# Kernel optimization log

Measured on AMD Instinct MI355X. Metric: run time of the kernel, lower is better.

Reference implementation:

```python
import jax, jax.numpy as jnp
import numpy as np
from jax.scipy.stats import norm

B, IN, H0, H1, OUT = 1024, 2048, 4096, 4096, 1000
EPS_CDF = 1e-5
DECAY = 0.01
NEG_SLOPE = 0.01  # LeakyReLU default slope


def setup_inputs() -> dict:
    key = jax.random.key(0)
    ks = iter(jax.random.split(key, 40))
    rn = lambda shp, s=1.0: s * jax.random.normal(next(ks), shp, dtype=jnp.float32)
    inp = {}
    inp['x'] = rn((B, IN))
    inp['z_w'] = rn((IN,), 0.02)
    for nm, (o, i) in zip(['0', '1', 'o'], [(H0, IN), (H1, H0), (OUT, H1)]):
        inp['w_mu' + nm] = rn((o, i), 0.02)
        inp['w_ls' + nm] = rn((o, i), 0.1) - 2.0  # log-sigma ~ -2 => sigma ~ 0.13
        inp['b_mu' + nm] = rn((o,), 0.02)
        inp['b_ls' + nm] = rn((o,), 0.1) - 2.0
        inp['eps_w' + nm] = rn((o, i))
        inp['eps_b' + nm] = rn((o,))
    inp['pfz0'] = jax.random.uniform(next(ks), (B, H0), dtype=jnp.float32)
    inp['pfz1'] = jax.random.uniform(next(ks), (B, H1), dtype=jnp.float32)
    inp['y'] = jax.random.randint(next(ks), (B,), 0, OUT, dtype=jnp.int32)
    inp['mz0'] = jax.random.randint(next(ks), (B, H0), 0, 2, dtype=jnp.int32)
    inp['mz1'] = jax.random.randint(next(ks), (B, H1), 0, 2, dtype=jnp.int32)
    inp['mask_mu0'] = jax.random.randint(next(ks), (H0,), 0, 2, dtype=jnp.int32)
    inp['mask_mu1'] = jax.random.randint(next(ks), (H1,), 0, 2, dtype=jnp.int32)
    inp['data_set_size'] = 60000
    return inp


def _bayes_layer(h, w_mu, w_ls, b_mu, b_ls, eps_w, eps_b, mz, mask_mu, pfz):
    sw = jnp.exp(w_ls)
    sb = jnp.exp(b_ls)
    w = w_mu + sw * eps_w          # reparameterized weight sample
    b = b_mu + sb * eps_b
    h = h @ w.T + b                # F.linear
    h = jnp.where(h >= 0, h, NEG_SLOPE * h)  # LeakyReLU
    mzf = mz.astype(h.dtype)
    m = mzf * mask_mu.astype(h.dtype)[None, :]   # [B, h]
    mult = m.shape[1] / (m.sum(1) + 1e-6)        # rescale multiplier per sample
    h = h * m * mult[:, None]
    # GFN forward-flow log-prob of the z-mask
    p = jnp.clip(pfz, 1e-6, 1.0 - 1e-6)
    flow = (mzf * jnp.log(p) + (1.0 - mzf) * jnp.log(1.0 - p)).sum()
    # Gaussian CDF likelihood of sampled weights/biases (finite-difference density)
    pw = norm.cdf(w + EPS_CDF, w_mu, sw) - norm.cdf(w - EPS_CDF, w_mu, sw)
    pb = norm.cdf(b + EPS_CDF, b_mu, sb) - norm.cdf(b - EPS_CDF, b_mu, sb)
    flow = flow + jnp.log(pw).sum() + jnp.log(pb).sum()
    return h, flow


def reference(x, z_w, w_mu0, w_ls0, b_mu0, b_ls0, eps_w0, eps_b0,
              w_mu1, w_ls1, b_mu1, b_ls1, eps_w1, eps_b1,
              w_muo, w_lso, b_muo, b_lso, eps_wo, eps_bo,
              pfz0, pfz1, y, mz0, mz1, mask_mu0, mask_mu1, data_set_size):
    loss = (x @ z_w).sum()  # total flow estimator Z
    h, f0 = _bayes_layer(x, w_mu0, w_ls0, b_mu0, b_ls0, eps_w0, eps_b0, mz0, mask_mu0, pfz0)
    loss = loss + f0
    h, f1 = _bayes_layer(h, w_mu1, w_ls1, b_mu1, b_ls1, eps_w1, eps_b1, mz1, mask_mu1, pfz1)
    loss = loss + f1
    # output BayesLinear (sampled)
    wo = w_muo + jnp.exp(w_lso) * eps_wo
    bo = b_muo + jnp.exp(b_lso) * eps_bo
    pred = h @ wo.T + bo  # [B, OUT]
    logp = jax.nn.log_softmax(pred, axis=-1)
    ce = -jnp.take_along_axis(logp, y[:, None].astype(jnp.int32), axis=1).mean()
    loss = loss + jnp.float32(data_set_size) * ce  # NLL
    wd = DECAY * ((w_mu0 ** 2).sum() + jnp.exp(w_ls0).sum()
                  + (w_mu1 ** 2).sum() + jnp.exp(w_ls1).sum())
    loss = (loss + wd) ** 2
    return pred, loss
```

## Files before the change

### kernel.cpp

```cpp
#include <hip/hip_runtime.h>
#include <math.h>

#define B_SZ 1024
#define IN_SZ 2048
#define H0_SZ 4096
#define H1_SZ 4096
#define OUT_SZ 1000

typedef _Float16 f16;
typedef __attribute__((ext_vector_type(4))) _Float16 f16x4;
typedef __attribute__((ext_vector_type(8))) _Float16 f16x8;
typedef __attribute__((ext_vector_type(4))) float f32x4;

#define OFF_N0     0ULL
#define OFF_N1     4ULL
#define OFF_MSUM0  256ULL
#define OFF_MSUM1  4352ULL
#define OFF_CPOS0  8448ULL
#define OFF_CPOS1  24832ULL
#define OFF_IDX0   41216ULL
#define OFF_IDX1   57600ULL
#define OFF_PXZ    73984ULL
#define OFF_PFL    82176ULL
#define OFF_PCE    98560ULL
#define OFF_PB     106752ULL
#define OFF_PW     107776ULL
#define OFF_BS0    370688ULL
#define OFF_BS1    387072ULL
#define OFF_BSO    403456ULL
#define OFF_XH     407552ULL
#define OFF_XL     4601856ULL
#define OFF_H0H    8796160ULL
#define OFF_H0L    17184768ULL
#define OFF_H1H    25573376ULL
#define OFF_H1L    33961984ULL
#define OFF_W0CH   42350592ULL
#define OFF_W0CL   59127808ULL
#define OFF_W1CH   75905024ULL
#define OFF_W1CL   109459456ULL
#define OFF_WOCH   143013888ULL
#define OFF_WOCL   151402496ULL
#define OFF_PART   159791104ULL

#define PSTRIDE_H  2560
#define PSTRIDE_O  1024

#define P0_IDX  2
#define P0_SX   258
#define P0_FL0  514
#define P0_FL1  770
#define P0_B0   786
#define P0_B1   802
#define P0_BO   806
#define L0_G    640
#define L0_W1   1664
#define L1_G    640
#define L1_WO   890

__device__ __forceinline__ void gload_lds16(const void* g, void* l)
{
    __builtin_amdgcn_global_load_lds((const __attribute__((address_space(1))) void*)g,
                                     (__attribute__((address_space(3))) void*)l, 16, 0, 0);
}

__device__ __forceinline__ void reduce4_store(double v0, double v1, double v2, double v3,
                                              double* dst)
{
    __shared__ double sh[4][4];
    double v[4] = {v0, v1, v2, v3};
    int lane = threadIdx.x & 63, wid = threadIdx.x >> 6;
#pragma unroll
    for (int a = 0; a < 4; ++a) {
        double x = v[a];
#pragma unroll
        for (int o = 32; o > 0; o >>= 1) x += __shfl_down(x, o, 64);
        if (lane == 0) sh[a][wid] = x;
    }
    __syncthreads();
    if (threadIdx.x == 0) {
        dst[0] = sh[0][0] + sh[0][1] + sh[0][2] + sh[0][3];
        dst[1] = sh[1][0] + sh[1][1] + sh[1][2] + sh[1][3];
        dst[2] = sh[2][0] + sh[2][1] + sh[2][2] + sh[2][3];
        dst[3] = sh[3][0] + sh[3][1] + sh[3][2] + sh[3][3];
    }
}

__device__ __forceinline__ void reduce1_store(double v, double* dst)
{
    __shared__ double sh1[4];
    int lane = threadIdx.x & 63, wid = threadIdx.x >> 6;
#pragma unroll
    for (int o = 32; o > 0; o >>= 1) v += __shfl_down(v, o, 64);
    if (lane == 0) sh1[wid] = v;
    __syncthreads();
    if (threadIdx.x == 0) dst[0] = sh1[0] + sh1[1] + sh1[2] + sh1[3];
}

__device__ void role_idx256(int pass,
                            const int* __restrict__ mask0, const int* __restrict__ mask1,
                            int* __restrict__ cpos0, int* __restrict__ idx0, int* __restrict__ n0,
                            int* __restrict__ cpos1, int* __restrict__ idx1, int* __restrict__ n1)
{
    __shared__ int sh[256];
    const int t = threadIdx.x;
    const int* mask = pass ? mask1 : mask0;
    int* cpos = pass ? cpos1 : cpos0;
    int* idx = pass ? idx1 : idx0;
    int* np = pass ? n1 : n0;
    const int4* m4 = (const int4*)mask;
    int4 q[4];
#pragma unroll
    for (int jj = 0; jj < 4; ++jj) q[jj] = m4[t * 4 + jj];
    int s = 0;
#pragma unroll
    for (int jj = 0; jj < 4; ++jj) s += q[jj].x + q[jj].y + q[jj].z + q[jj].w;
    sh[t] = s;
    __syncthreads();
    for (int o = 1; o < 256; o <<= 1) {
        int v = (t >= o) ? sh[t - o] : 0;
        __syncthreads();
        sh[t] += v;
        __syncthreads();
    }
    int run = sh[t] - s;
#pragma unroll
    for (int jj = 0; jj < 4; ++jj) {
        int4 m = q[jj];
        int4 cp;
        cp.x = run; cp.y = run + m.x; cp.z = cp.y + m.y; cp.w = cp.z + m.z;
        ((int4*)cpos)[t * 4 + jj] = cp;
        const int e = 16 * t + 4 * jj;
        if (m.x) idx[cp.x] = e + 0;
        if (m.y) idx[cp.y] = e + 1;
        if (m.z) idx[cp.z] = e + 2;
        if (m.w) idx[cp.w] = e + 3;
        run = cp.w + m.w;
    }
    if (t == 255) *np = sh[255];
}


__device__ void role_splitx(int rb, const float4* x, const float4* zw,
                            f16x4* xh, f16x4* xl, double* pxz)
{
    const int n4 = B_SZ * IN_SZ / 4;
    double s = 0;
    int i = rb * 256 + threadIdx.x;
    const int stride = 256 * 256;
    for (; i < n4; i += stride) {
        float4 v = x[i];
        float4 z = zw[i & (IN_SZ / 4 - 1)];
        s += (double)((v.x * z.x + v.y * z.y) + (v.z * z.z + v.w * z.w));
        f16 h0 = (f16)v.x, h1 = (f16)v.y, h2 = (f16)v.z, h3 = (f16)v.w;
        f16x4 hv = {h0, h1, h2, h3};
        f16x4 lv = {(f16)(v.x - (float)h0), (f16)(v.y - (float)h1),
                    (f16)(v.z - (float)h2), (f16)(v.w - (float)h3)};
        xh[i] = hv; xl[i] = lv;
    }
    reduce1_store(s, pxz + rb);
}

__device__ void role_flow4(int bb, const int* mz, const float* pfz, const int* maskmu,
                           float* msum, double* pfl)
{
    const int w = threadIdx.x >> 6, lane = threadIdx.x & 63;
    const int r = bb * 4 + w;
    const int4* m4 = (const int4*)(mz + (size_t)r * 4096);
    const float4* p4 = (const float4*)(pfz + (size_t)r * 4096);
    const int4* k4 = (const int4*)maskmu;
    int s = 0;
    double fl = 0;
    for (int i = lane; i < 1024; i += 64) {
        int4 m = m4[i];
        float4 p = p4[i];
        int4 k = k4[i];
        s += m.x * k.x + m.y * k.y + m.z * k.z + m.w * k.w;
        float a0 = fminf(fmaxf(p.x, 1e-6f), 1.0f - 1e-6f);
        float a1 = fminf(fmaxf(p.y, 1e-6f), 1.0f - 1e-6f);
        float a2 = fminf(fmaxf(p.z, 1e-6f), 1.0f - 1e-6f);
        float a3 = fminf(fmaxf(p.w, 1e-6f), 1.0f - 1e-6f);
        float g0 = logf(m.x ? a0 : 1.0f - a0);
        float g1 = logf(m.y ? a1 : 1.0f - a1);
        float g2 = logf(m.z ? a2 : 1.0f - a2);
        float g3 = logf(m.w ? a3 : 1.0f - a3);
        fl += (double)((g0 + g1) + (g2 + g3));
    }
#pragma unroll
    for (int o = 32; o > 0; o >>= 1) s += __shfl_down(s, o, 64);
    if (lane == 0) msum[r] = (float)s;
    reduce1_store(fl, pfl + bb);
}

template <int RED>
__device__ void role_bsample(int rb, const float* bmu, const float* bls, const float* beps,
                             float* out, int n, double* pb)
{
    int i = rb * 256 + threadIdx.x;
    float l = 0.f, e = 0.f;
    if (i < n) {
        l = bls[i]; e = beps[i];
        out[i] = fmaf(__expf(l), e, bmu[i]);
    }
    if (RED) {
        double sls = (i < n) ? (double)l : 0.0;
        double se2 = (i < n) ? (double)e * e : 0.0;
        reduce4_store(sls, se2, 0.0, 0.0, pb + (size_t)rb * 4);
    }
}

__device__ void role_w04(int bb, const float* mu, const float* ls, const float* eps,
                         const int* maskR, const int* cposR, f16* hi, double* pw)
{
    double sls = 0, se2 = 0, smu2 = 0, sex = 0;
#pragma unroll
    for (int rr = 0; rr < 4; ++rr) {
        const int r = bb * 4 + rr;
        const size_t rbb = (size_t)r * IN_SZ;
        const float4* m4 = (const float4*)(mu + rbb);
        const float4* l4 = (const float4*)(ls + rbb);
        const float4* e4 = (const float4*)(eps + rbb);
        const bool wr_ = maskR[r] != 0;
        const int drow = cposR[r];
        f16* hrow = hi + (size_t)drow * IN_SZ;
        for (int i = threadIdx.x; i < IN_SZ / 4; i += 256) {
            float4 m = m4[i], l = l4[i], e = e4[i];
            float g0 = __expf(l.x), g1 = __expf(l.y), g2 = __expf(l.z), g3 = __expf(l.w);
            float w0 = fmaf(g0, e.x, m.x), w1 = fmaf(g1, e.y, m.y);
            float w2 = fmaf(g2, e.z, m.z), w3 = fmaf(g3, e.w, m.w);
            sls += (double)((l.x + l.y) + (l.z + l.w));
            se2 += (double)((e.x * e.x + e.y * e.y) + (e.z * e.z + e.w * e.w));
            smu2 += (double)((m.x * m.x + m.y * m.y) + (m.z * m.z + m.w * m.w));
            sex += (double)((g0 + g1) + (g2 + g3));
            if (wr_) {
                f16x4 hv = {(f16)w0, (f16)w1, (f16)w2, (f16)w3};
                *(f16x4*)(hrow + i * 4) = hv;
            }
        }
    }
    reduce4_store(sls, se2, smu2, sex, pw + (size_t)bb * 4);
}

template <int ROWC, int RED>
__device__ void role_colc4(int bb, const float* mu, const float* ls, const float* eps,
                           const int* maskR, const int* cposR,
                           const int* maskC, const int* cposC, const int* pNc,
                           f16* hi, double* pw, f16* ldsH)
{
    const int t = threadIdx.x;
    const f16x8 z8 = {0, 0, 0, 0, 0, 0, 0, 0};
    for (int i = t; i < 512; i += 256) ((f16x8*)ldsH)[i] = z8;
    __syncthreads();
    double sls = 0, se2 = 0, smu2 = 0, sex = 0;
    const int n8 = ((*pNc + 127) >> 7) << 4;
#pragma unroll
    for (int rr = 0; rr < 4; ++rr) {
        const int r = bb * 4 + rr;
        const size_t rbb = (size_t)r * 4096;
        const float4* m4 = (const float4*)(mu + rbb);
        const float4* l4 = (const float4*)(ls + rbb);
        const float4* e4 = (const float4*)(eps + rbb);
        const bool wr_ = ROWC ? (maskR[r] != 0) : true;
        const int drow = ROWC ? cposR[r] : r;
        for (int i = t; i < 1024; i += 256) {
            float4 m = m4[i], l = l4[i], e = e4[i];
            float g0 = __expf(l.x), g1 = __expf(l.y), g2 = __expf(l.z), g3 = __expf(l.w);
            float w0 = fmaf(g0, e.x, m.x), w1 = fmaf(g1, e.y, m.y);
            float w2 = fmaf(g2, e.z, m.z), w3 = fmaf(g3, e.w, m.w);
            if (RED) {
                sls += (double)((l.x + l.y) + (l.z + l.w));
                se2 += (double)((e.x * e.x + e.y * e.y) + (e.z * e.z + e.w * e.w));
                smu2 += (double)((m.x * m.x + m.y * m.y) + (m.z * m.z + m.w * m.w));
                sex += (double)((g0 + g1) + (g2 + g3));
            }
            if (wr_) {
                int4 mc = ((const int4*)maskC)[i];
                int4 cp = ((const int4*)cposC)[i];
                if (mc.x) ldsH[cp.x] = (f16)w0;
                if (mc.y) ldsH[cp.y] = (f16)w1;
                if (mc.z) ldsH[cp.z] = (f16)w2;
                if (mc.w) ldsH[cp.w] = (f16)w3;
            }
        }
        __syncthreads();
        if (wr_) {
            f16x8* hd = (f16x8*)(hi + (size_t)drow * 4096);
            for (int i = t; i < n8; i += 256) hd[i] = ((const f16x8*)ldsH)[i];
        }
        __syncthreads();
    }
    if (RED) reduce4_store(sls, se2, smu2, sex, pw + (size_t)bb * 4);
}

template <int NSPLIT>
__device__ void gemm_body(int bid, f16* ldsbase,
                          const f16* Ah, const f16* Al, int SA,
                          const f16* Wh, int SW,
                          const int* pN, int NFIX, const int* pK, int KFIX,
                          float* P0, float* P1, float* P2, float* P3,
                          float* P4, float* P5, float* P6, float* P7, int pstride)
{
    const int c8 = bid & 7, j = bid >> 3;
    int nt, mt, z;
    if (NSPLIT == 4) {
        const int p = c8 + 8 * (j % 10);
        nt = p >> 2; z = p & 3; mt = j / 10;
    } else {
        const int p = c8 + 8 * (j & 7);
        nt = p >> 3; z = p & 7; mt = j >> 3;
    }
    const int nvalid = pN ? *pN : NFIX;
    const int bn = nt * 128;
    if (bn >= nvalid) return;
    const int bm = mt * 128;
    const int kvalid = pK ? *pK : KFIX;
    const int ktiles = (kvalid + 31) >> 5;
    const int prt = (ktiles + NSPLIT - 1) / NSPLIT;
    const int kt0 = z * prt;
    const int kt1 = min(ktiles, kt0 + prt);
    float* Cf = (z == 0) ? P0 : (z == 1) ? P1 : (z == 2) ? P2 : (z == 3) ? P3
              : (z == 4) ? P4 : (z == 5) ? P5 : (z == 6) ? P6 : P7;

    const int tid = threadIdx.x;
    const int wv = tid >> 6, lane = tid & 63;
    const int wr = wv >> 1, wc = wv & 1;
    const int l15 = lane & 15, l4 = lane >> 4;

    const f16* sg[6];
    int ldst[6];
#pragma unroll
    for (int i = 0; i < 6; ++i) {
        const int c = wv * 6 + i;
        const int plane = c >> 3, cidx = c & 7;
        const f16* base = (plane == 0) ? Ah : (plane == 1) ? Al : Wh;
        const int S_ = (plane < 2) ? SA : SW;
        const int rowb = (plane < 2) ? bm : bn;
        sg[i] = base + (size_t)(rowb + cidx * 16 + l15) * S_ + l4 * 8;
        ldst[i] = c * 512 + lane * 8;
    }

#define STAGE(KT, B) do { \
        _Pragma("unroll") \
        for (int i_ = 0; i_ < 6; ++i_) \
            gload_lds16(sg[i_] + (size_t)(KT) * 32, ldsbase + (B) * 12288 + ldst[i_]); \
    } while (0)

    f32x4 acc[4][4];
#pragma unroll
    for (int m = 0; m < 4; ++m)
#pragma unroll
        for (int n = 0; n < 4; ++n) acc[m][n] = (f32x4){0.f, 0.f, 0.f, 0.f};

    if (kt0 < kt1) {
        STAGE(kt0, 0);
        int cur = 0;
        for (int kt = kt0; kt < kt1; ++kt) {
            asm volatile("s_waitcnt vmcnt(0)" ::: "memory");
            __builtin_amdgcn_s_barrier();
            __builtin_amdgcn_sched_barrier(0);
            if (kt + 1 < kt1) STAGE(kt + 1, cur ^ 1);
            __builtin_amdgcn_sched_barrier(0);
            const f16* L = ldsbase + cur * 12288;
            f16x8 ah[4], al[4], wh[4];
#pragma unroll
            for (int m = 0; m < 4; ++m) {
                ah[m] = *(const f16x8*)(L + (wr * 4 + m) * 512 + lane * 8);
                al[m] = *(const f16x8*)(L + 4096 + (wr * 4 + m) * 512 + lane * 8);
            }
#pragma unroll
            for (int n = 0; n < 4; ++n)
                wh[n] = *(const f16x8*)(L + 8192 + (wc * 4 + n) * 512 + lane * 8);
            __builtin_amdgcn_s_setprio(1);
#pragma unroll
            for (int m = 0; m < 4; ++m)
#pragma unroll
                for (int n = 0; n < 4; ++n)
                    acc[m][n] = __builtin_amdgcn_mfma_f32_16x16x32_f16(ah[m], wh[n], acc[m][n], 0, 0, 0);
#pragma unroll
            for (int m = 0; m < 4; ++m)
#pragma unroll
                for (int n = 0; n < 4; ++n)
                    acc[m][n] = __builtin_amdgcn_mfma_f32_16x16x32_f16(al[m], wh[n], acc[m][n], 0, 0, 0);
            __builtin_amdgcn_s_setprio(0);
            cur ^= 1;
        }
    }
#undef STAGE

#pragma unroll
    for (int n = 0; n < 4; ++n) {
        const int c = bn + wc * 64 + n * 16 + l15;
        if (c >= pstride) continue;
#pragma unroll
        for (int m = 0; m < 4; ++m)
#pragma unroll
            for (int j2 = 0; j2 < 4; ++j2) {
                const int row = bm + wr * 64 + m * 16 + l4 * 4 + j2;
                Cf[(size_t)row * pstride + c] = acc[m][n][j2];
            }
    }
}

__global__ __launch_bounds__(256) void pre0_kernel(
    const float* __restrict__ x, const float* __restrict__ zw,
    const float* __restrict__ bmu0, const float* __restrict__ bls0, const float* __restrict__ beps0,
    const float* __restrict__ bmu1, const float* __restrict__ bls1, const float* __restrict__ beps1,
    const float* __restrict__ bmuo, const float* __restrict__ blso, const float* __restrict__ bepso,
    const float* __restrict__ pfz0, const float* __restrict__ pfz1,
    const int* __restrict__ mz0, const int* __restrict__ mz1,
    const int* __restrict__ mmu0, const int* __restrict__ mmu1,
    int* __restrict__ cpos0, int* __restrict__ idx0, int* __restrict__ n0p,
    int* __restrict__ cpos1, int* __restrict__ idx1, int* __restrict__ n1p,
    f16* __restrict__ xh, f16* __restrict__ xl,
    float* __restrict__ bs0, float* __restrict__ bs1, float* __restrict__ bso,
    float* __restrict__ msum0, float* __restrict__ msum1,
    double* __restrict__ PXZ, double* __restrict__ PFL, double* __restrict__ PB)
{
    const int b = blockIdx.x;
    if (b < P0_IDX) {
        role_idx256(b, mmu0, mmu1, cpos0, idx0, n0p, cpos1, idx1, n1p);
    } else if (b < P0_SX) {
        role_splitx(b - P0_IDX, (const float4*)x, (const float4*)zw,
                    (f16x4*)xh, (f16x4*)xl, PXZ);
    } else if (b < P0_FL0) {
        role_flow4(b - P0_SX, mz0, pfz0, mmu0, msum0, PFL);
    } else if (b < P0_FL1) {
        role_flow4(b - P0_FL0, mz1, pfz1, mmu1, msum1, PFL + 1024);
    } else if (b < P0_B0) {
        role_bsample<1>(b - P0_FL1, bmu0, bls0, beps0, bs0, H0_SZ, PB);
    } else if (b < P0_B1) {
        role_bsample<1>(b - P0_B0, bmu1, bls1, beps1, bs1, H1_SZ, PB + 16 * 4);
    } else {
        role_bsample<0>(b - P0_B1, bmuo, blso, bepso, bso, OUT_SZ, nullptr);
    }
}

__global__ __launch_bounds__(256) void prepW0_kernel(
    const float* __restrict__ wmu0, const float* __restrict__ wls0, const float* __restrict__ weps0,
    const int* __restrict__ mmu0, const int* __restrict__ cpos0,
    f16* __restrict__ w0ch, double* __restrict__ PW)
{
    role_w04(blockIdx.x, wmu0, wls0, weps0, mmu0, cpos0, w0ch, PW);
}

__global__ __launch_bounds__(256, 3) void gemmL0_kernel(
    const f16* __restrict__ xh, const f16* __restrict__ xl, const f16* __restrict__ w0ch,
    const int* __restrict__ n0p,
    float* __restrict__ A0, float* __restrict__ A1,
    float* __restrict__ A2, float* __restrict__ A3,
    const float* __restrict__ wmu1, const float* __restrict__ wls1, const float* __restrict__ weps1,
    const int* __restrict__ mmu0, const int* __restrict__ mmu1,
    const int* __restrict__ cpos0, const int* __restrict__ cpos1,
    f16* __restrict__ w1ch, double* __restrict__ PW)
{
    __shared__ __align__(16) f16 lds[2][12288];
    const int b = blockIdx.x;
    if (b < L0_G) {
        gemm_body<4>(b, &lds[0][0], xh, xl, IN_SZ, w0ch, IN_SZ, n0p, 0, nullptr, IN_SZ,
                     A0, A1, A2, A3, nullptr, nullptr, nullptr, nullptr, PSTRIDE_H);
    } else {
        role_colc4<1, 1>(b - L0_G, wmu1, wls1, weps1, mmu1, cpos1, mmu0, cpos0, n0p,
                         w1ch, PW + (size_t)4096 * 4, &lds[0][0]);
    }
}

__global__ __launch_bounds__(256, 3) void gemmL1_kernel(
    const f16* __restrict__ h0h, const f16* __restrict__ h0l, const f16* __restrict__ w1ch,
    const int* __restrict__ n1p, const int* __restrict__ n0p,
    float* __restrict__ B0, float* __restrict__ B1,
    float* __restrict__ B2, float* __restrict__ B3,
    const float* __restrict__ wmuo, const float* __restrict__ wlso, const float* __restrict__ wepso,
    const int* __restrict__ mmu1, const int* __restrict__ cpos1,
    f16* __restrict__ woch)
{
    __shared__ __align__(16) f16 lds[2][12288];
    const int b = blockIdx.x;
    if (b < L1_G) {
        gemm_body<4>(b, &lds[0][0], h0h, h0l, 4096, w1ch, 4096, n1p, 0, n0p, 0,
                     B0, B1, B2, B3, nullptr, nullptr, nullptr, nullptr, PSTRIDE_H);
    } else {
        role_colc4<0, 0>(b - L1_G, wmuo, wlso, wepso, nullptr, nullptr, mmu1, cpos1, n1p,
                         woch, nullptr, &lds[0][0]);
    }
}

__global__ __launch_bounds__(256, 3) void gemmLo_kernel(
    const f16* __restrict__ h1h, const f16* __restrict__ h1l, const f16* __restrict__ woch,
    const int* __restrict__ n1p,
    float* __restrict__ Q0, float* __restrict__ Q1, float* __restrict__ Q2, float* __restrict__ Q3,
    float* __restrict__ Q4, float* __restrict__ Q5, float* __restrict__ Q6, float* __restrict__ Q7)
{
    __shared__ __align__(16) f16 lds[2][12288];
    gemm_body<8>(blockIdx.x, &lds[0][0], h1h, h1l, 4096, woch, 4096, nullptr, OUT_SZ, n1p, 0,
                 Q0, Q1, Q2, Q3, Q4, Q5, Q6, Q7, PSTRIDE_O);
}

__global__ __launch_bounds__(256) void combine4_kernel(
    const float* __restrict__ PA, const float* __restrict__ PB,
    const float* __restrict__ PC, const float* __restrict__ PD, int pstride,
    const float* __restrict__ bsamp, const int* __restrict__ idx,
    const int* __restrict__ mz, const float* __restrict__ msum,
    const int* __restrict__ pN,
    f16* __restrict__ Chh, f16* __restrict__ Chl)
{
    const int nv = *pN;
    const int bn = blockIdx.x * 64;
    const int bm = blockIdx.y * 64;
    const int t = threadIdx.x;
    const int c0 = bn + (t & 15) * 4;
    const int r0 = bm + (t >> 4);
#pragma unroll
    for (int rr = 0; rr < 4; ++rr) {
        const int row = r0 + rr * 16;
        const float mult = 4096.0f / (msum[row] + 1e-6f);
        float sv[4] = {0.f, 0.f, 0.f, 0.f};
        if (c0 < pstride) {
            float4 a = *(const float4*)(PA + (size_t)row * pstride + c0);
            float4 b = *(const float4*)(PB + (size_t)row * pstride + c0);
            float4 c = *(const float4*)(PC + (size_t)row * pstride + c0);
            float4 d = *(const float4*)(PD + (size_t)row * pstride + c0);
            sv[0] = (a.x + b.x) + (c.x + d.x);
            sv[1] = (a.y + b.y) + (c.y + d.y);
            sv[2] = (a.z + b.z) + (c.z + d.z);
            sv[3] = (a.w + b.w) + (c.w + d.w);
        }
        f16 hh[4], ll[4];
#pragma unroll
        for (int jj = 0; jj < 4; ++jj) {
            const int c = c0 + jj;
            float v = 0.f;
            if (c < nv) {
                const int orig = idx[c];
                v = sv[jj] + bsamp[orig];
                v = v >= 0.f ? v : 0.01f * v;
                v = v * (float)mz[(size_t)row * 4096 + orig] * mult;
            }
            hh[jj] = (f16)v;
            ll[jj] = (f16)(v - (float)hh[jj]);
        }
        f16x4 hv = {hh[0], hh[1], hh[2], hh[3]};
        f16x4 lv = {ll[0], ll[1], ll[2], ll[3]};
        *(f16x4*)(Chh + (size_t)row * 4096 + c0) = hv;
        *(f16x4*)(Chl + (size_t)row * 4096 + c0) = lv;
    }
}

__global__ __launch_bounds__(256) void ce_fused8_kernel(
    const float* __restrict__ Q0, const float* __restrict__ Q1,
    const float* __restrict__ Q2, const float* __restrict__ Q3,
    const float* __restrict__ Q4, const float* __restrict__ Q5,
    const float* __restrict__ Q6, const float* __restrict__ Q7,
    const float* __restrict__ bso, const int* __restrict__ y,
    float* __restrict__ pred, double* __restrict__ pce)
{
    const int b = blockIdx.x;
    float mx = -1e30f;
    for (int jj = threadIdx.x; jj < OUT_SZ; jj += 256) {
        const size_t o = (size_t)b * PSTRIDE_O + jj;
        float v = ((Q0[o] + Q1[o]) + (Q2[o] + Q3[o]))
                + ((Q4[o] + Q5[o]) + (Q6[o] + Q7[o])) + bso[jj];
        pred[(size_t)b * OUT_SZ + jj] = v;
        mx = fmaxf(mx, v);
    }
#pragma unroll
    for (int o = 32; o > 0; o >>= 1) mx = fmaxf(mx, __shfl_down(mx, o, 64));
    __shared__ float sm[4];
    if ((threadIdx.x & 63) == 0) sm[threadIdx.x >> 6] = mx;
    __syncthreads();
    mx = fmaxf(fmaxf(sm[0], sm[1]), fmaxf(sm[2], sm[3]));
    double se = 0;
    for (int jj = threadIdx.x; jj < OUT_SZ; jj += 256)
        se += (double)__expf(pred[(size_t)b * OUT_SZ + jj] - mx);
#pragma unroll
    for (int o = 32; o > 0; o >>= 1) se += __shfl_down(se, o, 64);
    __shared__ double sd[4];
    if ((threadIdx.x & 63) == 0) sd[threadIdx.x >> 6] = se;
    __syncthreads();
    if (threadIdx.x == 0) {
        double lse = (double)mx + log(sd[0] + sd[1] + sd[2] + sd[3]);
        pce[b] = lse - (double)pred[(size_t)b * OUT_SZ + y[b]];
    }
}

__global__ __launch_bounds__(256) void finalize_kernel(
    const double* __restrict__ PXZ, const double* __restrict__ PFL,
    const double* __restrict__ PCE, const double* __restrict__ PB,
    const double* __restrict__ PW, const int* __restrict__ dss, float* __restrict__ out)
{
    const int t = threadIdx.x;
    double xz = 0, fl = 0, ce = 0, ls = 0, e2 = 0, mu2 = 0, ex = 0;
    xz += PXZ[t];
    fl += PFL[t] + PFL[1024 + t];
    for (int i = t; i < 1024; i += 256) ce += PCE[i];
    for (int i = t; i < 1024; i += 256) {
        const double* p0 = PW + (size_t)i * 4;
        const double* p1 = PW + (size_t)(4096 + i) * 4;
        ls += p0[0] + p1[0];
        e2 += p0[1] + p1[1];
        mu2 += p0[2] + p1[2];
        ex += p0[3] + p1[3];
    }
    if (t < 32) { ls += PB[t * 4]; e2 += PB[t * 4 + 1]; }
    __shared__ double sh[7][4];
    double v[7] = {xz, fl, ce, ls, e2, mu2, ex};
    const int lane = t & 63, wid = t >> 6;
#pragma unroll
    for (int a = 0; a < 7; ++a) {
        double x = v[a];
#pragma unroll
        for (int o = 32; o > 0; o >>= 1) x += __shfl_down(x, o, 64);
        if (lane == 0) sh[a][wid] = x;
    }
    __syncthreads();
    if (t == 0) {
        double T[7];
#pragma unroll
        for (int a = 0; a < 7; ++a) T[a] = sh[a][0] + sh[a][1] + sh[a][2] + sh[a][3];
        const double NTOT = 25174016.0;
        double cst = NTOT * (log(2.0e-5) - 0.91893853320467274178);
        double loss = T[0]
                    + cst - T[3] - 0.5 * T[4]
                    + T[1]
                    + (double)(*dss) * (T[2] / (double)B_SZ)
                    + 0.01 * (T[5] + T[6]);
        out[(size_t)B_SZ * OUT_SZ] = (float)(loss * loss);
    }
}

extern "C" void kernel_launch(void* const* d_in, const int* in_sizes, int n_in,
                              void* d_out, int out_size, void* d_ws, size_t ws_size,
                              hipStream_t stream)
{
    const float* x = (const float*)d_in[0];
    const float* zw = (const float*)d_in[1];
    const float* wmu0 = (const float*)d_in[2];
    const float* wls0 = (const float*)d_in[3];
    const float* bmu0 = (const float*)d_in[4];
    const float* bls0 = (const float*)d_in[5];
    const float* weps0 = (const float*)d_in[6];
    const float* beps0 = (const float*)d_in[7];
    const float* wmu1 = (const float*)d_in[8];
    const float* wls1 = (const float*)d_in[9];
    const float* bmu1 = (const float*)d_in[10];
    const float* bls1 = (const float*)d_in[11];
    const float* weps1 = (const float*)d_in[12];
    const float* beps1 = (const float*)d_in[13];
    const float* wmuo = (const float*)d_in[14];
    const float* wlso = (const float*)d_in[15];
    const float* bmuo = (const float*)d_in[16];
    const float* blso = (const float*)d_in[17];
    const float* wepso = (const float*)d_in[18];
    const float* bepso = (const float*)d_in[19];
    const float* pfz0 = (const float*)d_in[20];
    const float* pfz1 = (const float*)d_in[21];
    const int* y = (const int*)d_in[22];
    const int* mz0 = (const int*)d_in[23];
    const int* mz1 = (const int*)d_in[24];
    const int* mmu0 = (const int*)d_in[25];
    const int* mmu1 = (const int*)d_in[26];
    const int* dss = (const int*)d_in[27];

    char* ws = (char*)d_ws;
    int* n0p = (int*)(ws + OFF_N0);
    int* n1p = (int*)(ws + OFF_N1);
    float* msum0 = (float*)(ws + OFF_MSUM0);
    float* msum1 = (float*)(ws + OFF_MSUM1);
    int* cpos0 = (int*)(ws + OFF_CPOS0);
    int* cpos1 = (int*)(ws + OFF_CPOS1);
    int* idx0 = (int*)(ws + OFF_IDX0);
    int* idx1 = (int*)(ws + OFF_IDX1);
    double* PXZ = (double*)(ws + OFF_PXZ);
    double* PFL = (double*)(ws + OFF_PFL);
    double* PCE = (double*)(ws + OFF_PCE);
    double* PB = (double*)(ws + OFF_PB);
    double* PW = (double*)(ws + OFF_PW);
    float* bs0 = (float*)(ws + OFF_BS0);
    float* bs1 = (float*)(ws + OFF_BS1);
    float* bso = (float*)(ws + OFF_BSO);
    f16* xh = (f16*)(ws + OFF_XH);
    f16* xl = (f16*)(ws + OFF_XL);
    f16* h0h = (f16*)(ws + OFF_H0H);
    f16* h0l = (f16*)(ws + OFF_H0L);
    f16* h1h = (f16*)(ws + OFF_H1H);
    f16* h1l = (f16*)(ws + OFF_H1L);
    f16* w0ch = (f16*)(ws + OFF_W0CH);
    f16* w1ch = (f16*)(ws + OFF_W1CH);
    f16* woch = (f16*)(ws + OFF_WOCH);
    float* out = (float*)d_out;

    float* A0 = (float*)(ws + OFF_H1H);
    float* A1 = (float*)(ws + OFF_PART);
    float* A2 = (float*)(ws + OFF_W0CL);
    float* A3 = (float*)(ws + OFF_W1CL);
    float* B0 = (float*)(ws + OFF_W0CH);
    float* B1 = (float*)(ws + OFF_W0CL);
    float* B2 = (float*)(ws + OFF_W1CL);
    float* B3 = (float*)(ws + OFF_PART);
    float* Q[8];
    for (int i = 0; i < 8; ++i) Q[i] = (float*)(ws + OFF_W0CH + (size_t)i * 4194304ULL);

    pre0_kernel<<<P0_BO, 256, 0, stream>>>(
        x, zw, bmu0, bls0, beps0, bmu1, bls1, beps1, bmuo, blso, bepso,
        pfz0, pfz1, mz0, mz1, mmu0, mmu1,
        cpos0, idx0, n0p, cpos1, idx1, n1p,
        xh, xl, bs0, bs1, bso, msum0, msum1, PXZ, PFL, PB);

    prepW0_kernel<<<1024, 256, 0, stream>>>(
        wmu0, wls0, weps0, mmu0, cpos0, w0ch, PW);

    gemmL0_kernel<<<L0_W1, 256, 0, stream>>>(
        xh, xl, w0ch, n0p, A0, A1, A2, A3,
        wmu1, wls1, weps1, mmu0, mmu1, cpos0, cpos1,
        w1ch, PW);
    combine4_kernel<<<dim3(40, 16), 256, 0, stream>>>(
        A0, A1, A2, A3, PSTRIDE_H, bs0, idx0, mz0, msum0, n0p, h0h, h0l);

    gemmL1_kernel<<<L1_WO, 256, 0, stream>>>(
        h0h, h0l, w1ch, n1p, n0p, B0, B1, B2, B3,
        wmuo, wlso, wepso, mmu1, cpos1, woch);
    combine4_kernel<<<dim3(40, 16), 256, 0, stream>>>(
        B0, B1, B2, B3, PSTRIDE_H, bs1, idx1, mz1, msum1, n1p, h1h, h1l);

    gemmLo_kernel<<<512, 256, 0, stream>>>(
        h1h, h1l, woch, n1p, Q[0], Q[1], Q[2], Q[3], Q[4], Q[5], Q[6], Q[7]);

    ce_fused8_kernel<<<B_SZ, 256, 0, stream>>>(Q[0], Q[1], Q[2], Q[3], Q[4], Q[5], Q[6], Q[7],
                                               bso, y, out, PCE);
    finalize_kernel<<<1, 256, 0, stream>>>(PXZ, PFL, PCE, PB, PW, dss, out);
}
```

Before: 256.2 us.

## Fold W0 sampling into pre-kernel with gathered rows and shrink GEMM M-tile

Sampling of the layer-0 weights moves into the pre0 kernel and is written uncompacted, so the separate prepW0 launch and its dependency on the compaction indices go away. The layer-0 GEMM instead gathers weight rows through idx0 at load time. All GEMMs switch from 128x128 to 64x128 tiles with less LDS, an occupancy hint raised to 5, and doubled grids. The cost is converting all 4096 W0 rows rather than only the active ones, plus extra W reloads because the M tile is smaller.

Result: slower. 265.4 us (+3.6%).

```diff
diff --git a/kernel.cpp b/kernel.cpp
--- a/kernel.cpp
+++ b/kernel.cpp
@@ -46,16 +46,17 @@
 #define PSTRIDE_O  1024
 
 #define P0_IDX  2
-#define P0_SX   258
-#define P0_FL0  514
-#define P0_FL1  770
-#define P0_B0   786
-#define P0_B1   802
-#define P0_BO   806
-#define L0_G    640
-#define L0_W1   1664
-#define L1_G    640
-#define L1_WO   890
+#define P0_W0   1026
+#define P0_SX   1282
+#define P0_FL0  1538
+#define P0_FL1  1794
+#define P0_B0   1810
+#define P0_B1   1826
+#define P0_BO   1830
+#define L0_G    1280
+#define L0_W1   2304
+#define L1_G    1280
+#define L1_WO   1530
 
 __device__ __forceinline__ void gload_lds16(const void* g, void* l)
 {
@@ -208,8 +209,8 @@
     }
 }
 
-__device__ void role_w04(int bb, const float* mu, const float* ls, const float* eps,
-                         const int* maskR, const int* cposR, f16* hi, double* pw)
+__device__ void role_w0f4(int bb, const float* mu, const float* ls, const float* eps,
+                          f16* hi, double* pw)
 {
     double sls = 0, se2 = 0, smu2 = 0, sex = 0;
 #pragma unroll
@@ -219,9 +220,7 @@
         const float4* m4 = (const float4*)(mu + rbb);
         const float4* l4 = (const float4*)(ls + rbb);
         const float4* e4 = (const float4*)(eps + rbb);
-        const bool wr_ = maskR[r] != 0;
-        const int drow = cposR[r];
-        f16* hrow = hi + (size_t)drow * IN_SZ;
+        f16* hrow = hi + (size_t)r * IN_SZ;
         for (int i = threadIdx.x; i < IN_SZ / 4; i += 256) {
             float4 m = m4[i], l = l4[i], e = e4[i];
             float g0 = __expf(l.x), g1 = __expf(l.y), g2 = __expf(l.z), g3 = __expf(l.w);
@@ -231,10 +230,8 @@
             se2 += (double)((e.x * e.x + e.y * e.y) + (e.z * e.z + e.w * e.w));
             smu2 += (double)((m.x * m.x + m.y * m.y) + (m.z * m.z + m.w * m.w));
             sex += (double)((g0 + g1) + (g2 + g3));
-            if (wr_) {
-                f16x4 hv = {(f16)w0, (f16)w1, (f16)w2, (f16)w3};
-                *(f16x4*)(hrow + i * 4) = hv;
-            }
+            f16x4 hv = {(f16)w0, (f16)w1, (f16)w2, (f16)w3};
+            *(f16x4*)(hrow + i * 4) = hv;
         }
     }
     reduce4_store(sls, se2, smu2, sex, pw + (size_t)bb * 4);
@@ -294,7 +291,7 @@
 template <int NSPLIT>
 __device__ void gemm_body(int bid, f16* ldsbase,
                           const f16* Ah, const f16* Al, int SA,
-                          const f16* Wh, int SW,
+                          const f16* Wh, int SW, const int* widx,
                           const int* pN, int NFIX, const int* pK, int KFIX,
                           float* P0, float* P1, float* P2, float* P3,
                           float* P4, float* P5, float* P6, float* P7, int pstride)
@@ -311,7 +308,7 @@
     const int nvalid = pN ? *pN : NFIX;
     const int bn = nt * 128;
     if (bn >= nvalid) return;
-    const int bm = mt * 128;
+    const int bm = mt * 64;
     const int kvalid = pK ? *pK : KFIX;
     const int ktiles = (kvalid + 31) >> 5;
     const int prt = (ktiles + NSPLIT - 1) / NSPLIT;
@@ -325,28 +322,30 @@
     const int wr = wv >> 1, wc = wv & 1;
     const int l15 = lane & 15, l4 = lane >> 4;
 
-    const f16* sg[6];
-    int ldst[6];
-#pragma unroll
-    for (int i = 0; i < 6; ++i) {
-        const int c = wv * 6 + i;
-        const int plane = c >> 3, cidx = c & 7;
-        const f16* base = (plane == 0) ? Ah : (plane == 1) ? Al : Wh;
-        const int S_ = (plane < 2) ? SA : SW;
-        const int rowb = (plane < 2) ? bm : bn;
-        sg[i] = base + (size_t)(rowb + cidx * 16 + l15) * S_ + l4 * 8;
+    const f16* sg[4];
+    int ldst[4];
+#pragma unroll
+    for (int i = 0; i < 4; ++i) {
+        const int c = wv * 4 + i;
+        const f16* base; int rowb, S_, cidx, isW;
+        if (c < 4)      { base = Ah; rowb = bm; S_ = SA; cidx = c;     isW = 0; }
+        else if (c < 8) { base = Al; rowb = bm; S_ = SA; cidx = c - 4; isW = 0; }
+        else            { base = Wh; rowb = bn; S_ = SW; cidx = c - 8; isW = 1; }
+        int row = rowb + cidx * 16 + l15;
+        if (isW && widx) row = (row < nvalid) ? widx[row] : 0;
+        sg[i] = base + (size_t)row * S_ + l4 * 8;
         ldst[i] = c * 512 + lane * 8;
     }
 
 #define STAGE(KT, B) do { \
         _Pragma("unroll") \
-        for (int i_ = 0; i_ < 6; ++i_) \
-            gload_lds16(sg[i_] + (size_t)(KT) * 32, ldsbase + (B) * 12288 + ldst[i_]); \
+        for (int i_ = 0; i_ < 4; ++i_) \
+            gload_lds16(sg[i_] + (size_t)(KT) * 32, ldsbase + (B) * 8192 + ldst[i_]); \
     } while (0)
 
-    f32x4 acc[4][4];
-#pragma unroll
-    for (int m = 0; m < 4; ++m)
+    f32x4 acc[2][4];
+#pragma unroll
+    for (int m = 0; m < 2; ++m)
 #pragma unroll
         for (int n = 0; n < 4; ++n) acc[m][n] = (f32x4){0.f, 0.f, 0.f, 0.f};
 
@@ -359,24 +358,24 @@
             __builtin_amdgcn_sched_barrier(0);
             if (kt + 1 < kt1) STAGE(kt + 1, cur ^ 1);
             __builtin_amdgcn_sched_barrier(0);
-            const f16* L = ldsbase + cur * 12288;
-            f16x8 ah[4], al[4], wh[4];
-#pragma unroll
-            for (int m = 0; m < 4; ++m) {
-                ah[m] = *(const f16x8*)(L + (wr * 4 + m) * 512 + lane * 8);
-                al[m] = *(const f16x8*)(L + 4096 + (wr * 4 + m) * 512 + lane * 8);
+            const f16* L = ldsbase + cur * 8192;
+            f16x8 ah[2], al[2], wh[4];
+#pragma unroll
+            for (int m = 0; m < 2; ++m) {
+                ah[m] = *(const f16x8*)(L + (wr * 2 + m) * 512 + lane * 8);
+                al[m] = *(const f16x8*)(L + 2048 + (wr * 2 + m) * 512 + lane * 8);
             }
 #pragma unroll
             for (int n = 0; n < 4; ++n)
-                wh[n] = *(const f16x8*)(L + 8192 + (wc * 4 + n) * 512 + lane * 8);
+                wh[n] = *(const f16x8*)(L + 4096 + (wc * 4 + n) * 512 + lane * 8);
             __builtin_amdgcn_s_setprio(1);
 #pragma unroll
-            for (int m = 0; m < 4; ++m)
+            for (int m = 0; m < 2; ++m)
 #pragma unroll
                 for (int n = 0; n < 4; ++n)
                     acc[m][n] = __builtin_amdgcn_mfma_f32_16x16x32_f16(ah[m], wh[n], acc[m][n], 0, 0, 0);
 #pragma unroll
-            for (int m = 0; m < 4; ++m)
+            for (int m = 0; m < 2; ++m)
 #pragma unroll
                 for (int n = 0; n < 4; ++n)
                     acc[m][n] = __builtin_amdgcn_mfma_f32_16x16x32_f16(al[m], wh[n], acc[m][n], 0, 0, 0);
@@ -391,10 +390,10 @@
         const int c = bn + wc * 64 + n * 16 + l15;
         if (c >= pstride) continue;
 #pragma unroll
-        for (int m = 0; m < 4; ++m)
+        for (int m = 0; m < 2; ++m)
 #pragma unroll
             for (int j2 = 0; j2 < 4; ++j2) {
-                const int row = bm + wr * 64 + m * 16 + l4 * 4 + j2;
+                const int row = bm + wr * 32 + m * 16 + l4 * 4 + j2;
                 Cf[(size_t)row * pstride + c] = acc[m][n][j2];
             }
     }
@@ -402,6 +401,7 @@
 
 __global__ __launch_bounds__(256) void pre0_kernel(
     const float* __restrict__ x, const float* __restrict__ zw,
+    const float* __restrict__ wmu0, const float* __restrict__ wls0, const float* __restrict__ weps0,
     const float* __restrict__ bmu0, const float* __restrict__ bls0, const float* __restrict__ beps0,
     const float* __restrict__ bmu1, const float* __restrict__ bls1, const float* __restrict__ beps1,
     const float* __restrict__ bmuo, const float* __restrict__ blso, const float* __restrict__ bepso,
@@ -410,16 +410,19 @@
     const int* __restrict__ mmu0, const int* __restrict__ mmu1,
     int* __restrict__ cpos0, int* __restrict__ idx0, int* __restrict__ n0p,
     int* __restrict__ cpos1, int* __restrict__ idx1, int* __restrict__ n1p,
-    f16* __restrict__ xh, f16* __restrict__ xl,
+    f16* __restrict__ xh, f16* __restrict__ xl, f16* __restrict__ w0full,
     float* __restrict__ bs0, float* __restrict__ bs1, float* __restrict__ bso,
     float* __restrict__ msum0, float* __restrict__ msum1,
-    double* __restrict__ PXZ, double* __restrict__ PFL, double* __restrict__ PB)
+    double* __restrict__ PXZ, double* __restrict__ PFL,
+    double* __restrict__ PB, double* __restrict__ PW)
 {
     const int b = blockIdx.x;
     if (b < P0_IDX) {
         role_idx256(b, mmu0, mmu1, cpos0, idx0, n0p, cpos1, idx1, n1p);
+    } else if (b < P0_W0) {
+        role_w0f4(b - P0_IDX, wmu0, wls0, weps0, w0full, PW);
     } else if (b < P0_SX) {
-        role_splitx(b - P0_IDX, (const float4*)x, (const float4*)zw,
+        role_splitx(b - P0_W0, (const float4*)x, (const float4*)zw,
                     (f16x4*)xh, (f16x4*)xl, PXZ);
     } else if (b < P0_FL0) {
         role_flow4(b - P0_SX, mz0, pfz0, mmu0, msum0, PFL);
@@ -434,17 +437,9 @@
     }
 }
 
-__global__ __launch_bounds__(256) void prepW0_kernel(
-    const float* __restrict__ wmu0, const float* __restrict__ wls0, const float* __restrict__ weps0,
-    const int* __restrict__ mmu0, const int* __restrict__ cpos0,
-    f16* __restrict__ w0ch, double* __restrict__ PW)
-{
-    role_w04(blockIdx.x, wmu0, wls0, weps0, mmu0, cpos0, w0ch, PW);
-}
-
-__global__ __launch_bounds__(256, 3) void gemmL0_kernel(
-    const f16* __restrict__ xh, const f16* __restrict__ xl, const f16* __restrict__ w0ch,
-    const int* __restrict__ n0p,
+__global__ __launch_bounds__(256, 5) void gemmL0_kernel(
+    const f16* __restrict__ xh, const f16* __restrict__ xl, const f16* __restrict__ w0full,
+    const int* __restrict__ idx0, const int* __restrict__ n0p,
     float* __restrict__ A0, float* __restrict__ A1,
     float* __restrict__ A2, float* __restrict__ A3,
     const float* __restrict__ wmu1, const float* __restrict__ wls1, const float* __restrict__ weps1,
@@ -452,10 +447,11 @@
     const int* __restrict__ cpos0, const int* __restrict__ cpos1,
     f16* __restrict__ w1ch, double* __restrict__ PW)
 {
-    __shared__ __align__(16) f16 lds[2][12288];
+    __shared__ __align__(16) f16 lds[2][8192];
     const int b = blockIdx.x;
     if (b < L0_G) {
-        gemm_body<4>(b, &lds[0][0], xh, xl, IN_SZ, w0ch, IN_SZ, n0p, 0, nullptr, IN_SZ,
+        gemm_body<4>(b, &lds[0][0], xh, xl, IN_SZ, w0full, IN_SZ, idx0,
+                     n0p, 0, nullptr, IN_SZ,
                      A0, A1, A2, A3, nullptr, nullptr, nullptr, nullptr, PSTRIDE_H);
     } else {
         role_colc4<1, 1>(b - L0_G, wmu1, wls1, weps1, mmu1, cpos1, mmu0, cpos0, n0p,
@@ -463,7 +459,7 @@
     }
 }
 
-__global__ __launch_bounds__(256, 3) void gemmL1_kernel(
+__global__ __launch_bounds__(256, 5) void gemmL1_kernel(
     const f16* __restrict__ h0h, const f16* __restrict__ h0l, const f16* __restrict__ w1ch,
     const int* __restrict__ n1p, const int* __restrict__ n0p,
     float* __restrict__ B0, float* __restrict__ B1,
@@ -472,10 +468,11 @@
     const int* __restrict__ mmu1, const int* __restrict__ cpos1,
     f16* __restrict__ woch)
 {
-    __shared__ __align__(16) f16 lds[2][12288];
+    __shared__ __align__(16) f16 lds[2][8192];
     const int b = blockIdx.x;
     if (b < L1_G) {
-        gemm_body<4>(b, &lds[0][0], h0h, h0l, 4096, w1ch, 4096, n1p, 0, n0p, 0,
+        gemm_body<4>(b, &lds[0][0], h0h, h0l, 4096, w1ch, 4096, nullptr,
+                     n1p, 0, n0p, 0,
                      B0, B1, B2, B3, nullptr, nullptr, nullptr, nullptr, PSTRIDE_H);
     } else {
         role_colc4<0, 0>(b - L1_G, wmuo, wlso, wepso, nullptr, nullptr, mmu1, cpos1, n1p,
@@ -483,14 +480,15 @@
     }
 }
 
-__global__ __launch_bounds__(256, 3) void gemmLo_kernel(
+__global__ __launch_bounds__(256, 5) void gemmLo_kernel(
     const f16* __restrict__ h1h, const f16* __restrict__ h1l, const f16* __restrict__ woch,
     const int* __restrict__ n1p,
     float* __restrict__ Q0, float* __restrict__ Q1, float* __restrict__ Q2, float* __restrict__ Q3,
     float* __restrict__ Q4, float* __restrict__ Q5, float* __restrict__ Q6, float* __restrict__ Q7)
 {
-    __shared__ __align__(16) f16 lds[2][12288];
-    gemm_body<8>(blockIdx.x, &lds[0][0], h1h, h1l, 4096, woch, 4096, nullptr, OUT_SZ, n1p, 0,
+    __shared__ __align__(16) f16 lds[2][8192];
+    gemm_body<8>(blockIdx.x, &lds[0][0], h1h, h1l, 4096, woch, 4096, nullptr,
+                 nullptr, OUT_SZ, n1p, 0,
                  Q0, Q1, Q2, Q3, Q4, Q5, Q6, Q7, PSTRIDE_O);
 }
 
@@ -682,7 +680,7 @@
     f16* h0l = (f16*)(ws + OFF_H0L);
     f16* h1h = (f16*)(ws + OFF_H1H);
     f16* h1l = (f16*)(ws + OFF_H1L);
-    f16* w0ch = (f16*)(ws + OFF_W0CH);
+    f16* w0full = (f16*)(ws + OFF_W0CH);
     f16* w1ch = (f16*)(ws + OFF_W1CH);
     f16* woch = (f16*)(ws + OFF_WOCH);
     float* out = (float*)d_out;
@@ -699,16 +697,14 @@
     for (int i = 0; i < 8; ++i) Q[i] = (float*)(ws + OFF_W0CH + (size_t)i * 4194304ULL);
 
     pre0_kernel<<<P0_BO, 256, 0, stream>>>(
-        x, zw, bmu0, bls0, beps0, bmu1, bls1, beps1, bmuo, blso, bepso,
+        x, zw, wmu0, wls0, weps0,
+        bmu0, bls0, beps0, bmu1, bls1, beps1, bmuo, blso, bepso,
         pfz0, pfz1, mz0, mz1, mmu0, mmu1,
         cpos0, idx0, n0p, cpos1, idx1, n1p,
-        xh, xl, bs0, bs1, bso, msum0, msum1, PXZ, PFL, PB);
-
-    prepW0_kernel<<<1024, 256, 0, stream>>>(
-        wmu0, wls0, weps0, mmu0, cpos0, w0ch, PW);
+        xh, xl, w0full, bs0, bs1, bso, msum0, msum1, PXZ, PFL, PB, PW);
 
     gemmL0_kernel<<<L0_W1, 256, 0, stream>>>(
-        xh, xl, w0ch, n0p, A0, A1, A2, A3,
+        xh, xl, w0full, idx0, n0p, A0, A1, A2, A3,
         wmu1, wls1, weps1, mmu0, mmu1, cpos0, cpos1,
         w1ch, PW);
     combine4_kernel<<<dim3(40, 16), 256, 0, stream>>>(
@@ -720,7 +716,7 @@
     combine4_kernel<<<dim3(40, 16), 256, 0, stream>>>(
         B0, B1, B2, B3, PSTRIDE_H, bs1, idx1, mz1, msum1, n1p, h1h, h1l);
 
-    gemmLo_kernel<<<512, 256, 0, stream>>>(
+    gemmLo_kernel<<<1024, 256, 0, stream>>>(
         h1h, h1l, woch, n1p, Q[0], Q[1], Q[2], Q[3], Q[4], Q[5], Q[6], Q[7]);
 
     ce_fused8_kernel<<<B_SZ, 256, 0, stream>>>(Q[0], Q[1], Q[2], Q[3], Q[4], Q[5], Q[6], Q[7],
```
